# Kernel tuning notes

Hardware: AMD Instinct MI355X
Metric: run time of the kernel (lower is better)

The kernel has to match this reference:

```python
import jax, jax.numpy as jnp
import numpy as np
from jax import lax

GAMMA = 0.1


def setup_inputs() -> dict:
    key = jax.random.key(0)
    k1, k2 = jax.random.split(key)
    pred = jax.random.normal(k1, (64, 512), dtype=jnp.float32)
    target = jax.random.normal(k2, (64, 512), dtype=jnp.float32)
    return {"pred": pred, "target": target}


def _soft_dtw(pred, target, gamma=GAMMA):
    # pred, target: [B, L]
    B, L = pred.shape
    inf = jnp.float32(jnp.inf)
    # pairwise squared distances: [B, L, L]
    dist = (pred[:, :, None] - target[:, None, :]) ** 2

    def softmin3(r0, r1, r2):
        # -gamma * logsumexp(-r/gamma) over the 3 predecessors (stable)
        s = jnp.stack([r0, r1, r2], axis=-1)
        return -gamma * jax.nn.logsumexp(-s / gamma, axis=-1)

    # R[0, :] = [0, inf, inf, ...]  (row 0 of the (L+1)x(L+1) DP table)
    init_row = jnp.concatenate(
        [jnp.zeros((B, 1), jnp.float32), jnp.full((B, L), inf, jnp.float32)], axis=1
    )  # [B, L+1]

    def row_step(prev_row, d_row):
        # prev_row: R[i-1, :] of shape [B, L+1]; d_row: dist[:, i-1, :] of shape [B, L]
        r0s = prev_row[:, :-1].T  # R[i-1, j-1], [L, B]
        r1s = prev_row[:, 1:].T   # R[i-1, j],   [L, B]
        ds = d_row.T              # [L, B]

        def cell(r_left, inp):
            r0, r1, d = inp
            val = d + softmin3(r0, r1, r_left)
            return val, val

        _, vals = lax.scan(cell, jnp.full((B,), inf, jnp.float32), (r0s, r1s, ds))
        new_row = jnp.concatenate([jnp.full((B, 1), inf, jnp.float32), vals.T], axis=1)
        return new_row, None

    # scan over rows i = 1..L; dist reordered to [L, B, L]
    last_row, _ = lax.scan(row_step, init_row, jnp.swapaxes(dist, 0, 1))
    return last_row[:, -1].mean()  # R[:, L, L].mean()


def reference(pred, target):
    return _soft_dtw(pred, target)
```

## Files before the change

### kernel.cpp

```cpp
#include <hip/hip_runtime.h>

#define LSEQ 512
#define NB 64
#define NCHUNK 51

__device__ __forceinline__ float dpp_shr1_inj(float inj, float x) {
  return __int_as_float(__builtin_amdgcn_update_dpp(
      __float_as_int(inj), __float_as_int(x), 0x138, 0xF, 0xF, false));
}

__device__ __forceinline__ float rdlane(float x, int u) {
  return __int_as_float(__builtin_amdgcn_readlane(__float_as_int(x), u));
}

__device__ __forceinline__ float exp2_fast(float x) {
  const float xc = fmaxf(x, -126.0f);
  const float f = __builtin_fmaf(xc, 8388608.0f, 1065353216.0f);
  return __int_as_float((int)f);
}

template <bool FULL>
__device__ __forceinline__ void chunk16(
    int cbase, const float* tgpad, const float* ringP, float* ringW, float p0,
    float p1, bool is_wr, int lane, float& v0, float& v1, float& r0) {
  float tt[16];
  const int tb = 64 + cbase - lane;
#pragma unroll
  for (int k = 0; k < 16; ++k) tt[k] = tgpad[tb + k];

  const float rj = ringP[(cbase + 1 + (lane & 15)) & 127];
  float sj[16];
#pragma unroll
  for (int k = 0; k < 16; ++k) sj[k] = rdlane(rj, k);

  const float C23 = 1.1920929e-7f;
  float vv[16];
#pragma unroll
  for (int u = 0; u < 16; ++u) {
    const float r1 = dpp_shr1_inj(sj[u], v1);
    const float tcu = tt[u];
    const float diff0 = p0 - tcu;
    const float M0 = fminf(fminf(r0, r1), v0);
    const float md0 = __builtin_amdgcn_fmed3f(r0, r1, v0);
    const float mx0 = fmaxf(fmaxf(r0, r1), v0);
    const float e0 = 1.0f + (exp2_fast(M0 - md0) + exp2_fast(M0 - mx0));
    const float dm0 = __builtin_fmaf(diff0, diff0, M0);
    const float li0 = (float)(1064992256 - __float_as_int(e0));
    const float d0 = __builtin_fmaf(li0, C23, dm0);
    const float diff1 = p1 - tcu;
    const float M1 = fminf(fminf(v0, d0), v1);
    const float md1 = __builtin_amdgcn_fmed3f(v0, d0, v1);
    const float mx1 = fmaxf(fmaxf(v0, d0), v1);
    const float e1 = 1.0f + (exp2_fast(M1 - md1) + exp2_fast(M1 - mx1));
    const float dm1 = __builtin_fmaf(diff1, diff1, M1);
    const float li1 = (float)(1064992256 - __float_as_int(e1));
    const float d1 = __builtin_fmaf(li1, C23, dm1);
    vv[u] = d1;
    if (FULL) {
      v0 = d0;
      v1 = d1;
    } else {
      const int j = cbase + 1 + u - lane;
      const bool act = ((unsigned)(j - 1)) < (unsigned)LSEQ;
      v0 = act ? d0 : v0;
      v1 = act ? d1 : v1;
    }
    r0 = r1;
  }

  if (is_wr) {
    const int j0 = cbase - 62;
#pragma unroll
    for (int k = 0; k < 8; ++k) {
      if (FULL || (((unsigned)(j0 + 2 * k - 1)) < (unsigned)LSEQ))
        *(float2*)&ringW[(j0 + 2 * k) & 127] =
            make_float2(vv[2 * k], vv[2 * k + 1]);
      else if (((unsigned)(j0 + 2 * k)) < (unsigned)LSEQ)
        ringW[(j0 + 2 * k + 1) & 127] = vv[2 * k + 1];
    }
  }
}

__global__ __launch_bounds__(256) void dtw_band(
    const float* __restrict__ pred, const float* __restrict__ target,
    float* __restrict__ part) {
  const int b = blockIdx.x;
  const int tid = threadIdx.x;
  const int w = tid >> 6;
  const int lane = tid & 63;
  const bool is_wr = (lane == 63) && (w < 3);

  __shared__ float tgpad[640];
  __shared__ float rings[4][128];

  const float SC = 3.79828146f;
  const float2 pp = ((const float2*)(pred + b * LSEQ))[tid];
  const float p0 = pp.x * SC, p1 = pp.y * SC;
  const float2 tt = ((const float2*)(target + b * LSEQ))[tid];
  ((float2*)(tgpad + 64))[tid] = make_float2(tt.x * SC, tt.y * SC);
  if (tid < 64) {
    tgpad[tid] = 0.0f;
    tgpad[576 + tid] = 0.0f;
  }
  ((float2*)rings)[tid] = make_float2(INFINITY, INFINITY);

  const int lag = w * 80;
  const int cw0 = 5 * w;
  const float* __restrict__ ringP = rings[w == 0 ? 3 : w - 1];
  float* __restrict__ ringW = rings[w];

  float v0 = INFINITY;
  float v1 = INFINITY;
  float r0 = (tid == 0) ? 0.0f : INFINITY;

  for (int c = 0; c < NCHUNK; ++c) {
    __syncthreads();
    if (c < cw0 || c > cw0 + 35) continue;
    const int cbase = 16 * c - lag;
    if (c >= cw0 + 4 && c <= cw0 + 31)
      chunk16<true>(cbase, tgpad, ringP, ringW, p0, p1, is_wr, lane, v0, v1,
                    r0);
    else
      chunk16<false>(cbase, tgpad, ringP, ringW, p0, p1, is_wr, lane, v0, v1,
                     r0);
  }

  if (tid == 255)
    part[b] = v1 * 0.069314718f;
}

__global__ void dtw_reduce(const float* __restrict__ part,
                           float* __restrict__ out) {
  float v = part[threadIdx.x];
#pragma unroll
  for (int o = 32; o > 0; o >>= 1) v += __shfl_down(v, o);
  if (threadIdx.x == 0) out[0] = v * (1.0f / NB);
}

extern "C" void kernel_launch(void* const* d_in, const int* in_sizes, int n_in,
                              void* d_out, int out_size, void* d_ws,
                              size_t ws_size, hipStream_t stream) {
  const float* pred = (const float*)d_in[0];
  const float* target = (const float*)d_in[1];
  float* part = (float*)d_ws;

  dtw_band<<<NB, 256, 0, stream>>>(pred, target, part);
  dtw_reduce<<<1, 64, 0, stream>>>(part, (float*)d_out);
}
```

Measured before the change: 85.43 us.

## Assign one DP row per lane and use eight wavefronts per batch

Each lane now computes a single row of the soft-DTW table instead of two chained rows. The block grows from 256 to 512 threads: eight wavefronts, each covering 64 rows, are staggered by 80 columns and pass boundary values through eight LDS rings, with the chunk count raised to match. This removes the serial second-row step from each lane's inner loop, shortening the dependent chain per chunk. In exchange the pipeline has more chunks, more barriers, and a longer fill and drain time across eight waves.

```diff
diff --git a/kernel.cpp b/kernel.cpp
--- a/kernel.cpp
+++ b/kernel.cpp
@@ -2,7 +2,7 @@
 
 #define LSEQ 512
 #define NB 64
-#define NCHUNK 51
+#define NCHUNK 71
 
 __device__ __forceinline__ float dpp_shr1_inj(float inj, float x) {
   return __int_as_float(__builtin_amdgcn_update_dpp(
@@ -20,9 +20,10 @@
 }
 
 template <bool FULL>
-__device__ __forceinline__ void chunk16(
-    int cbase, const float* tgpad, const float* ringP, float* ringW, float p0,
-    float p1, bool is_wr, int lane, float& v0, float& v1, float& r0) {
+__device__ __forceinline__ void chunk16(int cbase, const float* tgpad,
+                                        const float* ringP, float* ringW,
+                                        float p, bool is_wr, int lane,
+                                        float& v, float& r0) {
   float tt[16];
   const int tb = 64 + cbase - lane;
 #pragma unroll
@@ -37,33 +38,22 @@
   float vv[16];
 #pragma unroll
   for (int u = 0; u < 16; ++u) {
-    const float r1 = dpp_shr1_inj(sj[u], v1);
-    const float tcu = tt[u];
-    const float diff0 = p0 - tcu;
-    const float M0 = fminf(fminf(r0, r1), v0);
-    const float md0 = __builtin_amdgcn_fmed3f(r0, r1, v0);
-    const float mx0 = fmaxf(fmaxf(r0, r1), v0);
-    const float e0 = 1.0f + (exp2_fast(M0 - md0) + exp2_fast(M0 - mx0));
-    const float dm0 = __builtin_fmaf(diff0, diff0, M0);
-    const float li0 = (float)(1064992256 - __float_as_int(e0));
-    const float d0 = __builtin_fmaf(li0, C23, dm0);
-    const float diff1 = p1 - tcu;
-    const float M1 = fminf(fminf(v0, d0), v1);
-    const float md1 = __builtin_amdgcn_fmed3f(v0, d0, v1);
-    const float mx1 = fmaxf(fmaxf(v0, d0), v1);
-    const float e1 = 1.0f + (exp2_fast(M1 - md1) + exp2_fast(M1 - mx1));
-    const float dm1 = __builtin_fmaf(diff1, diff1, M1);
-    const float li1 = (float)(1064992256 - __float_as_int(e1));
-    const float d1 = __builtin_fmaf(li1, C23, dm1);
-    vv[u] = d1;
+    const float r1 = dpp_shr1_inj(sj[u], v);
+    const float diff = p - tt[u];
+    const float M = fminf(fminf(r0, r1), v);
+    const float md = __builtin_amdgcn_fmed3f(r0, r1, v);
+    const float mx = fmaxf(fmaxf(r0, r1), v);
+    const float e = 1.0f + (exp2_fast(M - md) + exp2_fast(M - mx));
+    const float dm = __builtin_fmaf(diff, diff, M);
+    const float li = (float)(1064992256 - __float_as_int(e));
+    const float d = __builtin_fmaf(li, C23, dm);
+    vv[u] = d;
     if (FULL) {
-      v0 = d0;
-      v1 = d1;
+      v = d;
     } else {
       const int j = cbase + 1 + u - lane;
       const bool act = ((unsigned)(j - 1)) < (unsigned)LSEQ;
-      v0 = act ? d0 : v0;
-      v1 = act ? d1 : v1;
+      v = act ? d : v;
     }
     r0 = r1;
   }
@@ -81,23 +71,21 @@
   }
 }
 
-__global__ __launch_bounds__(256) void dtw_band(
+__global__ __launch_bounds__(512) void dtw_band(
     const float* __restrict__ pred, const float* __restrict__ target,
     float* __restrict__ part) {
   const int b = blockIdx.x;
   const int tid = threadIdx.x;
   const int w = tid >> 6;
   const int lane = tid & 63;
-  const bool is_wr = (lane == 63) && (w < 3);
+  const bool is_wr = (lane == 63) && (w < 7);
 
   __shared__ float tgpad[640];
-  __shared__ float rings[4][128];
+  __shared__ float rings[8][128];
 
   const float SC = 3.79828146f;
-  const float2 pp = ((const float2*)(pred + b * LSEQ))[tid];
-  const float p0 = pp.x * SC, p1 = pp.y * SC;
-  const float2 tt = ((const float2*)(target + b * LSEQ))[tid];
-  ((float2*)(tgpad + 64))[tid] = make_float2(tt.x * SC, tt.y * SC);
+  const float p = pred[b * LSEQ + tid] * SC;
+  tgpad[64 + tid] = target[b * LSEQ + tid] * SC;
   if (tid < 64) {
     tgpad[tid] = 0.0f;
     tgpad[576 + tid] = 0.0f;
@@ -106,11 +94,10 @@
 
   const int lag = w * 80;
   const int cw0 = 5 * w;
-  const float* __restrict__ ringP = rings[w == 0 ? 3 : w - 1];
+  const float* __restrict__ ringP = rings[w == 0 ? 7 : w - 1];
   float* __restrict__ ringW = rings[w];
 
-  float v0 = INFINITY;
-  float v1 = INFINITY;
+  float v = INFINITY;
   float r0 = (tid == 0) ? 0.0f : INFINITY;
 
   for (int c = 0; c < NCHUNK; ++c) {
@@ -118,15 +105,13 @@
     if (c < cw0 || c > cw0 + 35) continue;
     const int cbase = 16 * c - lag;
     if (c >= cw0 + 4 && c <= cw0 + 31)
-      chunk16<true>(cbase, tgpad, ringP, ringW, p0, p1, is_wr, lane, v0, v1,
-                    r0);
+      chunk16<true>(cbase, tgpad, ringP, ringW, p, is_wr, lane, v, r0);
     else
-      chunk16<false>(cbase, tgpad, ringP, ringW, p0, p1, is_wr, lane, v0, v1,
-                     r0);
+      chunk16<false>(cbase, tgpad, ringP, ringW, p, is_wr, lane, v, r0);
   }
 
-  if (tid == 255)
-    part[b] = v1 * 0.069314718f;
+  if (tid == 511)
+    part[b] = v * 0.069314718f;
 }
 
 __global__ void dtw_reduce(const float* __restrict__ part,
@@ -144,6 +129,6 @@
   const float* target = (const float*)d_in[1];
   float* part = (float*)d_ws;
 
-  dtw_band<<<NB, 256, 0, stream>>>(pred, target, part);
+  dtw_band<<<NB, 512, 0, stream>>>(pred, target, part);
   dtw_reduce<<<1, 64, 0, stream>>>(part, (float*)d_out);
 }
```

After: 100.5 us. 1.18x slower.
